# Kernel optimization log

Measured on AMD Instinct MI355X. Metric: run time of the kernel, lower is better.

The kernel has to match this reference:

```python
import jax, jax.numpy as jnp
import numpy as np

NUM_NODES = 50000
HIDDEN = 128
NUM_REL = 8
NUM_EDGES = 600000


def setup_inputs() -> dict:
    key = jax.random.key(0)
    ks = jax.random.split(key, 10)
    s = 1.0 / np.sqrt(HIDDEN)
    return {
        "edge_index": jax.random.randint(ks[0], (2, NUM_EDGES), 0, NUM_NODES, dtype=jnp.int32),
        "edge_type": jax.random.randint(ks[1], (NUM_EDGES,), 0, NUM_REL, dtype=jnp.int32),
        "node_emb": jax.random.normal(ks[2], (NUM_NODES, HIDDEN), jnp.float32),
        "W1": jax.random.normal(ks[3], (NUM_REL, HIDDEN, HIDDEN), jnp.float32) * s,
        "root1": jax.random.normal(ks[4], (HIDDEN, HIDDEN), jnp.float32) * s,
        "b1": jnp.zeros((HIDDEN,), jnp.float32),
        "W2": jax.random.normal(ks[5], (NUM_REL, HIDDEN, HIDDEN), jnp.float32) * s,
        "root2": jax.random.normal(ks[6], (HIDDEN, HIDDEN), jnp.float32) * s,
        "b2": jnp.zeros((HIDDEN,), jnp.float32),
    }


def rgcn_layer(x, W, root, bias, src, dst, rel):
    # PyG RGCNConv: per-relation MEAN aggregation of neighbor features,
    # transformed by relation weight, plus root transform and bias.
    N = x.shape[0]
    R = W.shape[0]
    # transform node features by every relation weight: [N, R, F]
    xw = jnp.einsum('nd,rdf->nrf', x, W)
    # per-(dst, relation) in-edge counts for mean normalization
    cnt = jnp.zeros((N, R), x.dtype).at[dst, rel].add(1.0)
    inv = 1.0 / jnp.maximum(cnt, 1.0)
    # per-edge message, normalized by destination's per-relation degree
    msg = xw[src, rel] * inv[dst, rel][:, None]  # [E, F]
    agg = jnp.zeros((N, W.shape[2]), x.dtype).at[dst].add(msg)
    return agg + x @ root + bias


def reference(edge_index, edge_type, node_emb, W1, root1, b1, W2, root2, b2):
    src, dst = edge_index[0], edge_index[1]
    h = jax.nn.relu(rgcn_layer(node_emb, W1, root1, b1, src, dst, edge_type))
    out = rgcn_layer(h, W2, root2, b2, src, dst, edge_type)
    return out
```

## Files before the change

### kernel.cpp

```cpp
#include <hip/hip_runtime.h>

#define H 128
#define RREL 8
#define NJ 9

typedef short bf16x8 __attribute__((ext_vector_type(8)));
typedef float f32x4 __attribute__((ext_vector_type(4)));
typedef unsigned short u16x8 __attribute__((ext_vector_type(8)));

static __device__ __forceinline__ unsigned short f2bf(float f) {
    unsigned int u = __float_as_uint(f);
    unsigned int r = (u + 0x7fffu + ((u >> 16) & 1u)) >> 16;
    return (unsigned short)r;
}
static __device__ __forceinline__ float bf2f(unsigned short u) {
    return __uint_as_float(((unsigned int)u) << 16);
}

__global__ void zero_kernel(int* p, long n) {
    long i = (long)blockIdx.x * blockDim.x + threadIdx.x;
    long stride = (long)gridDim.x * blockDim.x;
    for (; i < n; i += stride) p[i] = 0;
}

__global__ void count_kernel(const int* __restrict__ ei, const int* __restrict__ et,
                             int* __restrict__ cnt, int E) {
    int e = blockIdx.x * 256 + threadIdx.x;
    if (e >= E) return;
    int d = ei[E + e];
    int r = et[e];
    atomicAdd(&cnt[(size_t)d * RREL + r], 1);
}

__global__ void scan_block_kernel(const int* __restrict__ cnt, int* __restrict__ rploc,
                                  int* __restrict__ bsum, int N) {
    __shared__ int s[256];
    int t = threadIdx.x;
    int d = blockIdx.x * 256 + t;
    int v = 0;
    if (d < N) {
#pragma unroll
        for (int r = 0; r < RREL; ++r) v += cnt[(size_t)d * RREL + r];
    }
    s[t] = v;
    __syncthreads();
#pragma unroll
    for (int off = 1; off < 256; off <<= 1) {
        int u = 0;
        if (t >= off) u = s[t - off];
        __syncthreads();
        s[t] += u;
        __syncthreads();
    }
    if (d < N) rploc[d] = s[t] - v;
    if (t == 255) bsum[blockIdx.x] = s[255];
}

__global__ void scan_top_kernel(const int* __restrict__ bsum, int* __restrict__ boff, int nb) {
    __shared__ int s[256];
    int t = threadIdx.x;
    int v = (t < nb) ? bsum[t] : 0;
    s[t] = v;
    __syncthreads();
#pragma unroll
    for (int off = 1; off < 256; off <<= 1) {
        int u = 0;
        if (t >= off) u = s[t - off];
        __syncthreads();
        s[t] += u;
        __syncthreads();
    }
    boff[t] = s[t] - v;
}

__global__ void finalize_kernel(const int* __restrict__ cnt, const int* __restrict__ rploc,
                                const int* __restrict__ boff, int* __restrict__ rowptr2,
                                float* __restrict__ inv, int N) {
    int d = blockIdx.x * 256 + threadIdx.x;
    if (d >= N) return;
    int run = rploc[d] + boff[d >> 8];
#pragma unroll
    for (int r = 0; r < RREL; ++r) {
        int c = cnt[(size_t)d * RREL + r];
        rowptr2[(size_t)d * RREL + r] = run;
        inv[(size_t)d * RREL + r] = 1.0f / (float)max(c, 1);
        run += c;
    }
    if (d == N - 1) rowptr2[(size_t)N * RREL] = run;
}

__global__ void fill_kernel(const int* __restrict__ ei, const int* __restrict__ et,
                            int* __restrict__ cursor, const int* __restrict__ rowptr2,
                            int* __restrict__ ssrc, int E) {
    int e = blockIdx.x * 256 + threadIdx.x;
    if (e >= E) return;
    int d = ei[E + e];
    int r = et[e];
    int bin = d * RREL + r;
    int pos = rowptr2[bin] + atomicAdd(&cursor[bin], 1);
    ssrc[pos] = ei[e];
}

__global__ void tobf_kernel(const float* __restrict__ x, unsigned short* __restrict__ xb, long n) {
    long i = (long)blockIdx.x * blockDim.x + threadIdx.x;
    long stride = (long)gridDim.x * blockDim.x;
    for (; i < n; i += stride) xb[i] = f2bf(x[i]);
}

__global__ void wcat_kernel(const float* __restrict__ W1, const float* __restrict__ r1,
                            const float* __restrict__ W2, const float* __restrict__ r2,
                            unsigned short* __restrict__ WTa1, unsigned short* __restrict__ WTa2) {
    int id = blockIdx.x * 256 + threadIdx.x;
    const int per = NJ * H * H;
    if (id >= 2 * per) return;
    int b = id / per;
    int rem = id - b * per;
    int j = rem / (H * H);
    int fk = rem - j * (H * H);
    int f = fk >> 7, k = fk & 127;
    const float* W = b ? W2 : W1;
    const float* rt = b ? r2 : r1;
    float v = (j < RREL) ? W[((size_t)j * H + k) * H + f] : rt[(size_t)k * H + f];
    (b ? WTa2 : WTa1)[((size_t)j * H + f) * H + k] = f2bf(v);
}

__global__ __launch_bounds__(256) void xw_kernel(const unsigned short* __restrict__ xin,
                                                 const unsigned short* __restrict__ WTa,
                                                 unsigned short* __restrict__ Y,
                                                 int N, int j0, int j1) {
    __shared__ unsigned short Xs[64][136];
    __shared__ unsigned short Ws[128][136];
    const int t = threadIdx.x;
    const int w = t >> 6, l = t & 63;
    const int m_base = blockIdx.x * 64;
    const int colb = l & 15, quad = l >> 4;
    const u16x8 uz = {0, 0, 0, 0, 0, 0, 0, 0};
    const f32x4 fz = {0.f, 0.f, 0.f, 0.f};

#pragma unroll
    for (int p = 0; p < 4; ++p) {
        int c = p * 256 + t;
        int row = c >> 4, k8 = (c & 15) * 8;
        int gn = m_base + row;
        u16x8 v = uz;
        if (gn < N) v = *(const u16x8*)&xin[(size_t)gn * H + k8];
        *(u16x8*)&Xs[row][k8] = v;
    }

    for (int j = j0; j < j1; ++j) {
        __syncthreads();
#pragma unroll
        for (int p = 0; p < 8; ++p) {
            int c = p * 256 + t;
            int f = c >> 4, k8 = (c & 15) * 8;
            *(u16x8*)&Ws[f][k8] = *(const u16x8*)&WTa[((size_t)j * H + f) * H + k8];
        }
        __syncthreads();
        f32x4 acc[8];
#pragma unroll
        for (int n = 0; n < 8; ++n) acc[n] = fz;
#pragma unroll
        for (int ks = 0; ks < 4; ++ks) {
            int kl = ks * 32 + quad * 8;
            bf16x8 a = *(const bf16x8*)&Xs[w * 16 + colb][kl];
#pragma unroll
            for (int n = 0; n < 8; ++n) {
                bf16x8 b = *(const bf16x8*)&Ws[n * 16 + colb][kl];
                acc[n] = __builtin_amdgcn_mfma_f32_16x16x32_bf16(a, b, acc[n], 0, 0, 0);
            }
        }
        unsigned short* Yj = Y + (size_t)(j - j0) * N * H;
#pragma unroll
        for (int n = 0; n < 8; ++n) {
            int col = n * 16 + colb;
#pragma unroll
            for (int i = 0; i < 4; ++i) {
                int gn = m_base + w * 16 + quad * 4 + i;
                if (gn < N) Yj[(size_t)gn * H + col] = f2bf(acc[n][i]);
            }
        }
    }
}

__global__ __launch_bounds__(256) void gather_kernel(const unsigned short* __restrict__ Y,
                                                     const float* __restrict__ inv,
                                                     const int* __restrict__ rowptr2,
                                                     const int* __restrict__ ssrc,
                                                     const float* __restrict__ bias,
                                                     float* __restrict__ accf,
                                                     float* __restrict__ outf,
                                                     unsigned short* __restrict__ outb,
                                                     int N, int relu, int j0, int j1, int final_pass) {
    const int t = threadIdx.x;
    const int l = t & 63;
    int d = blockIdx.x * 16 + (t >> 4);
    if (d >= N) return;
    const int fl = l & 15;
    const int kc = fl * 8;
    int rp = 0;
    float ivl = 0.f;
    if (fl < 9) rp = rowptr2[(size_t)d * RREL + fl];
    if (fl < 8) ivl = inv[(size_t)d * RREL + fl];
    const int gbase = l & 48;
    float tot[8] = {};
    int rend = (j1 < RREL) ? j1 : RREL;
    for (int r = j0; r < rend; ++r) {
        int beg = __shfl(rp, gbase + r);
        int end = __shfl(rp, gbase + r + 1);
        float iv = __shfl(ivl, gbase + r);
        const unsigned short* Yr = Y + (size_t)(r - j0) * N * H;
        float af[8] = {};
        int i = beg;
        for (; i + 1 < end; i += 2) {
            int s0 = ssrc[i];
            int s1 = ssrc[i + 1];
            u16x8 v0 = *(const u16x8*)&Yr[(size_t)s0 * H + kc];
            u16x8 v1 = *(const u16x8*)&Yr[(size_t)s1 * H + kc];
#pragma unroll
            for (int j = 0; j < 8; ++j)
                af[j] += bf2f((unsigned short)v0[j]) + bf2f((unsigned short)v1[j]);
        }
        if (i < end) {
            int s0 = ssrc[i];
            u16x8 v0 = *(const u16x8*)&Yr[(size_t)s0 * H + kc];
#pragma unroll
            for (int j = 0; j < 8; ++j) af[j] += bf2f((unsigned short)v0[j]);
        }
#pragma unroll
        for (int j = 0; j < 8; ++j) tot[j] += af[j] * iv;
    }
    if (j1 == NJ) {
        u16x8 vr = *(const u16x8*)&Y[((size_t)(RREL - j0) * N + d) * H + kc];
#pragma unroll
        for (int j = 0; j < 8; ++j) tot[j] += bf2f((unsigned short)vr[j]);
    }
    if (j0 > 0) {
        f32x4 p0 = *(const f32x4*)&accf[(size_t)d * H + kc];
        f32x4 p1 = *(const f32x4*)&accf[(size_t)d * H + kc + 4];
#pragma unroll
        for (int j = 0; j < 4; ++j) { tot[j] += p0[j]; tot[4 + j] += p1[j]; }
    }
    if (final_pass) {
        f32x4 b0 = *(const f32x4*)&bias[kc];
        f32x4 b1 = *(const f32x4*)&bias[kc + 4];
#pragma unroll
        for (int j = 0; j < 4; ++j) { tot[j] += b0[j]; tot[4 + j] += b1[j]; }
        if (relu) {
#pragma unroll
            for (int j = 0; j < 8; ++j) tot[j] = fmaxf(tot[j], 0.f);
        }
        if (outf) {
            f32x4 o0, o1;
#pragma unroll
            for (int j = 0; j < 4; ++j) { o0[j] = tot[j]; o1[j] = tot[4 + j]; }
            *(f32x4*)&outf[(size_t)d * H + kc] = o0;
            *(f32x4*)&outf[(size_t)d * H + kc + 4] = o1;
        } else {
            u16x8 o;
#pragma unroll
            for (int j = 0; j < 8; ++j) o[j] = f2bf(tot[j]);
            *(u16x8*)&outb[(size_t)d * H + kc] = o;
        }
    } else {
        f32x4 o0, o1;
#pragma unroll
        for (int j = 0; j < 4; ++j) { o0[j] = tot[j]; o1[j] = tot[4 + j]; }
        *(f32x4*)&accf[(size_t)d * H + kc] = o0;
        *(f32x4*)&accf[(size_t)d * H + kc + 4] = o1;
    }
}

extern "C" void kernel_launch(void* const* d_in, const int* in_sizes, int n_in,
                              void* d_out, int out_size, void* d_ws, size_t ws_size,
                              hipStream_t stream) {
    const int* edge_index = (const int*)d_in[0];
    const int* edge_type  = (const int*)d_in[1];
    const float* node_emb = (const float*)d_in[2];
    const float* W1    = (const float*)d_in[3];
    const float* root1 = (const float*)d_in[4];
    const float* b1    = (const float*)d_in[5];
    const float* W2    = (const float*)d_in[6];
    const float* root2 = (const float*)d_in[7];
    const float* b2    = (const float*)d_in[8];
    float* out = (float*)d_out;

    const int E = in_sizes[1];
    const int N = in_sizes[2] / H;

    char* base = (char*)d_ws;
    size_t off = 0;
    auto take = [&](size_t bytes) { size_t o = off; off = (off + bytes + 63) & ~(size_t)63; return o; };
    int*   cnt     = (int*)  (base + take((size_t)N * RREL * 4));
    int*   cursor  = (int*)  (base + take((size_t)N * RREL * 4));
    int*   rploc   = (int*)  (base + take((size_t)N * 4));
    int*   bsum    = (int*)  (base + take(256 * 4));
    int*   boff    = (int*)  (base + take(256 * 4));
    int*   rowptr2 = (int*)  (base + take(((size_t)N * RREL + 1) * 4));
    float* inv     = (float*)(base + take((size_t)N * RREL * 4));
    int*   ssrc    = (int*)  (base + take((size_t)E * 4));
    unsigned short* WTa1 = (unsigned short*)(base + take((size_t)NJ * H * H * 2));
    unsigned short* WTa2 = (unsigned short*)(base + take((size_t)NJ * H * H * 2));
    unsigned short* xb  = (unsigned short*)(base + take((size_t)N * H * 2));
    unsigned short* hb  = (unsigned short*)(base + take((size_t)N * H * 2));

    size_t fixed_off = off;
    unsigned short* Y;
    float* accf = nullptr;
    int rc;
    size_t availA = (ws_size > fixed_off) ? ws_size - fixed_off : 0;
    if (availA >= (size_t)NJ * N * H * 2) {
        Y = (unsigned short*)(base + fixed_off);
        rc = NJ;
    } else {
        accf = (float*)(base + fixed_off);
        size_t off2 = fixed_off + (((size_t)N * H * 4 + 63) & ~(size_t)63);
        Y = (unsigned short*)(base + off2);
        size_t availB = (ws_size > off2) ? ws_size - off2 : 0;
        rc = (int)(availB / ((size_t)N * H * 2));
        if (rc > RREL) rc = RREL;
        if (rc < 1) rc = 1;
    }

    const int nbScan = (N + 255) / 256;

    zero_kernel<<<512, 256, 0, stream>>>(cnt, (long)N * RREL * 2);
    count_kernel<<<(E + 255) / 256, 256, 0, stream>>>(edge_index, edge_type, cnt, E);
    scan_block_kernel<<<nbScan, 256, 0, stream>>>(cnt, rploc, bsum, N);
    scan_top_kernel<<<1, 256, 0, stream>>>(bsum, boff, nbScan);
    finalize_kernel<<<nbScan, 256, 0, stream>>>(cnt, rploc, boff, rowptr2, inv, N);
    fill_kernel<<<(E + 255) / 256, 256, 0, stream>>>(edge_index, edge_type, cursor, rowptr2, ssrc, E);
    wcat_kernel<<<(2 * NJ * H * H + 255) / 256, 256, 0, stream>>>(W1, root1, W2, root2, WTa1, WTa2);
    tobf_kernel<<<1024, 256, 0, stream>>>(node_emb, xb, (long)N * H);

    const int gx = (N + 63) / 64;
    const int gg = (N + 15) / 16;

    auto run_layer = [&](const unsigned short* xin, const unsigned short* WTa, const float* bias,
                         float* of, unsigned short* ob, int relu) {
        for (int j0 = 0; j0 < NJ; j0 += rc) {
            int j1 = (j0 + rc < NJ) ? j0 + rc : NJ;
            int fin = (j1 == NJ);
            xw_kernel<<<gx, 256, 0, stream>>>(xin, WTa, Y, N, j0, j1);
            gather_kernel<<<gg, 256, 0, stream>>>(Y, inv, rowptr2, ssrc, bias, accf,
                                                  fin ? of : nullptr, fin ? ob : nullptr,
                                                  N, relu, j0, j1, fin);
        }
    };

    run_layer(xb, WTa1, b1, nullptr, hb, 1);
    run_layer(hb, WTa2, b2, out, nullptr, 0);
}
```

Baseline: 332.0 us.

## Pack edges per destination with relation bits, permute feature layout, widen xw tiles

Edges are now CSR-sorted by destination only, and each entry packs the relation id into the upper bits of the source index. The gather kernel loads 16 packed edges cooperatively and broadcasts them by shuffle, applying each edge's per-relation inverse degree. This replaces the per-(node,relation) loop with its many short, divergent segments. The xw kernel now computes 128 rows per block, reading A operands straight from global memory instead of staging them in LDS, and writes Y with 16-byte vector stores. To make those stores contiguous, the hidden dimension is permuted, which is undone through the permuted second-layer weights, the permuted bias and a strided final store. The costs are a per-edge relation check, uncoalesced A-operand loads, and a more fragile implicit layout contract between the two layers.

Measured after the change: 281.5 us. -15.2%, faster.

```diff
diff --git a/kernel.cpp b/kernel.cpp
--- a/kernel.cpp
+++ b/kernel.cpp
@@ -74,31 +74,30 @@
 }
 
 __global__ void finalize_kernel(const int* __restrict__ cnt, const int* __restrict__ rploc,
-                                const int* __restrict__ boff, int* __restrict__ rowptr2,
+                                const int* __restrict__ boff, int* __restrict__ rowptr,
                                 float* __restrict__ inv, int N) {
     int d = blockIdx.x * 256 + threadIdx.x;
     if (d >= N) return;
-    int run = rploc[d] + boff[d >> 8];
+    int rp = rploc[d] + boff[d >> 8];
+    rowptr[d] = rp;
+    int deg = 0;
 #pragma unroll
     for (int r = 0; r < RREL; ++r) {
         int c = cnt[(size_t)d * RREL + r];
-        rowptr2[(size_t)d * RREL + r] = run;
         inv[(size_t)d * RREL + r] = 1.0f / (float)max(c, 1);
-        run += c;
-    }
-    if (d == N - 1) rowptr2[(size_t)N * RREL] = run;
+        deg += c;
+    }
+    if (d == N - 1) rowptr[N] = rp + deg;
 }
 
 __global__ void fill_kernel(const int* __restrict__ ei, const int* __restrict__ et,
-                            int* __restrict__ cursor, const int* __restrict__ rowptr2,
-                            int* __restrict__ ssrc, int E) {
+                            int* __restrict__ cursor, const int* __restrict__ rowptr,
+                            int* __restrict__ packed, int E) {
     int e = blockIdx.x * 256 + threadIdx.x;
     if (e >= E) return;
     int d = ei[E + e];
-    int r = et[e];
-    int bin = d * RREL + r;
-    int pos = rowptr2[bin] + atomicAdd(&cursor[bin], 1);
-    ssrc[pos] = ei[e];
+    int pos = rowptr[d] + atomicAdd(&cursor[d], 1);
+    packed[pos] = ei[e] | (et[e] << 20);
 }
 
 __global__ void tobf_kernel(const float* __restrict__ x, unsigned short* __restrict__ xb, long n) {
@@ -109,43 +108,43 @@
 
 __global__ void wcat_kernel(const float* __restrict__ W1, const float* __restrict__ r1,
                             const float* __restrict__ W2, const float* __restrict__ r2,
-                            unsigned short* __restrict__ WTa1, unsigned short* __restrict__ WTa2) {
+                            const float* __restrict__ b1, const float* __restrict__ b2,
+                            unsigned short* __restrict__ WTa1, unsigned short* __restrict__ WTa2,
+                            float* __restrict__ biasP) {
     int id = blockIdx.x * 256 + threadIdx.x;
     const int per = NJ * H * H;
-    if (id >= 2 * per) return;
-    int b = id / per;
-    int rem = id - b * per;
-    int j = rem / (H * H);
-    int fk = rem - j * (H * H);
-    int f = fk >> 7, k = fk & 127;
-    const float* W = b ? W2 : W1;
-    const float* rt = b ? r2 : r1;
-    float v = (j < RREL) ? W[((size_t)j * H + k) * H + f] : rt[(size_t)k * H + f];
-    (b ? WTa2 : WTa1)[((size_t)j * H + f) * H + k] = f2bf(v);
+    if (id < per) {
+        int j = id / (H * H);
+        int fk = id - j * (H * H);
+        int f = fk >> 7, k = fk & 127;
+        float v = (j < RREL) ? W1[((size_t)j * H + k) * H + f] : r1[(size_t)k * H + f];
+        WTa1[id] = f2bf(v);
+        int ko = (k & 7) * 16 + (k >> 3);
+        float v2 = (j < RREL) ? W2[((size_t)j * H + ko) * H + f] : r2[(size_t)ko * H + f];
+        WTa2[id] = f2bf(v2);
+    } else if (id < per + 2 * H) {
+        int c = id - per;
+        int cp = c & 127;
+        int co = (cp & 7) * 16 + (cp >> 3);
+        biasP[c] = (c < H) ? b1[co] : b2[co];
+    }
 }
 
 __global__ __launch_bounds__(256) void xw_kernel(const unsigned short* __restrict__ xin,
                                                  const unsigned short* __restrict__ WTa,
                                                  unsigned short* __restrict__ Y,
                                                  int N, int j0, int j1) {
-    __shared__ unsigned short Xs[64][136];
     __shared__ unsigned short Ws[128][136];
     const int t = threadIdx.x;
     const int w = t >> 6, l = t & 63;
-    const int m_base = blockIdx.x * 64;
+    const int m_base = blockIdx.x * 128;
     const int colb = l & 15, quad = l >> 4;
-    const u16x8 uz = {0, 0, 0, 0, 0, 0, 0, 0};
     const f32x4 fz = {0.f, 0.f, 0.f, 0.f};
 
-#pragma unroll
-    for (int p = 0; p < 4; ++p) {
-        int c = p * 256 + t;
-        int row = c >> 4, k8 = (c & 15) * 8;
-        int gn = m_base + row;
-        u16x8 v = uz;
-        if (gn < N) v = *(const u16x8*)&xin[(size_t)gn * H + k8];
-        *(u16x8*)&Xs[row][k8] = v;
-    }
+    int row0 = m_base + w * 32 + colb;
+    int row1 = row0 + 16;
+    const unsigned short* xr0 = xin + (size_t)(row0 < N ? row0 : N - 1) * H;
+    const unsigned short* xr1 = xin + (size_t)(row1 < N ? row1 : N - 1) * H;
 
     for (int j = j0; j < j1; ++j) {
         __syncthreads();
@@ -156,27 +155,35 @@
             *(u16x8*)&Ws[f][k8] = *(const u16x8*)&WTa[((size_t)j * H + f) * H + k8];
         }
         __syncthreads();
-        f32x4 acc[8];
-#pragma unroll
-        for (int n = 0; n < 8; ++n) acc[n] = fz;
+        f32x4 acc[2][8];
+#pragma unroll
+        for (int mi = 0; mi < 2; ++mi)
+#pragma unroll
+            for (int n = 0; n < 8; ++n) acc[mi][n] = fz;
 #pragma unroll
         for (int ks = 0; ks < 4; ++ks) {
             int kl = ks * 32 + quad * 8;
-            bf16x8 a = *(const bf16x8*)&Xs[w * 16 + colb][kl];
+            bf16x8 a0 = *(const bf16x8*)&xr0[kl];
+            bf16x8 a1 = *(const bf16x8*)&xr1[kl];
 #pragma unroll
             for (int n = 0; n < 8; ++n) {
                 bf16x8 b = *(const bf16x8*)&Ws[n * 16 + colb][kl];
-                acc[n] = __builtin_amdgcn_mfma_f32_16x16x32_bf16(a, b, acc[n], 0, 0, 0);
+                acc[0][n] = __builtin_amdgcn_mfma_f32_16x16x32_bf16(a0, b, acc[0][n], 0, 0, 0);
+                acc[1][n] = __builtin_amdgcn_mfma_f32_16x16x32_bf16(a1, b, acc[1][n], 0, 0, 0);
             }
         }
         unsigned short* Yj = Y + (size_t)(j - j0) * N * H;
 #pragma unroll
-        for (int n = 0; n < 8; ++n) {
-            int col = n * 16 + colb;
+        for (int mi = 0; mi < 2; ++mi) {
 #pragma unroll
             for (int i = 0; i < 4; ++i) {
-                int gn = m_base + w * 16 + quad * 4 + i;
-                if (gn < N) Yj[(size_t)gn * H + col] = f2bf(acc[n][i]);
+                int row = m_base + w * 32 + mi * 16 + quad * 4 + i;
+                if (row < N) {
+                    u16x8 o;
+#pragma unroll
+                    for (int n = 0; n < 8; ++n) o[n] = f2bf(acc[mi][n][i]);
+                    *(u16x8*)&Yj[(size_t)row * H + colb * 8] = o;
+                }
             }
         }
     }
@@ -184,9 +191,9 @@
 
 __global__ __launch_bounds__(256) void gather_kernel(const unsigned short* __restrict__ Y,
                                                      const float* __restrict__ inv,
-                                                     const int* __restrict__ rowptr2,
-                                                     const int* __restrict__ ssrc,
-                                                     const float* __restrict__ bias,
+                                                     const int* __restrict__ rowptr,
+                                                     const int* __restrict__ packed,
+                                                     const float* __restrict__ biasP,
                                                      float* __restrict__ accf,
                                                      float* __restrict__ outf,
                                                      unsigned short* __restrict__ outb,
@@ -197,37 +204,48 @@
     if (d >= N) return;
     const int fl = l & 15;
     const int kc = fl * 8;
+    const int gbase = l & 48;
     int rp = 0;
+    if (fl < 2) rp = rowptr[d + fl];
     float ivl = 0.f;
-    if (fl < 9) rp = rowptr2[(size_t)d * RREL + fl];
     if (fl < 8) ivl = inv[(size_t)d * RREL + fl];
-    const int gbase = l & 48;
+    int beg = __shfl(rp, gbase);
+    int end = __shfl(rp, gbase + 1);
+    const int jr = (j1 < RREL) ? j1 : RREL;
     float tot[8] = {};
-    int rend = (j1 < RREL) ? j1 : RREL;
-    for (int r = j0; r < rend; ++r) {
-        int beg = __shfl(rp, gbase + r);
-        int end = __shfl(rp, gbase + r + 1);
-        float iv = __shfl(ivl, gbase + r);
-        const unsigned short* Yr = Y + (size_t)(r - j0) * N * H;
-        float af[8] = {};
-        int i = beg;
-        for (; i + 1 < end; i += 2) {
-            int s0 = ssrc[i];
-            int s1 = ssrc[i + 1];
-            u16x8 v0 = *(const u16x8*)&Yr[(size_t)s0 * H + kc];
-            u16x8 v1 = *(const u16x8*)&Yr[(size_t)s1 * H + kc];
-#pragma unroll
-            for (int j = 0; j < 8; ++j)
-                af[j] += bf2f((unsigned short)v0[j]) + bf2f((unsigned short)v1[j]);
-        }
-        if (i < end) {
-            int s0 = ssrc[i];
-            u16x8 v0 = *(const u16x8*)&Yr[(size_t)s0 * H + kc];
-#pragma unroll
-            for (int j = 0; j < 8; ++j) af[j] += bf2f((unsigned short)v0[j]);
-        }
-#pragma unroll
-        for (int j = 0; j < 8; ++j) tot[j] += af[j] * iv;
+    for (int i = beg; i < end; i += 16) {
+        int pk = (i + fl < end) ? packed[i + fl] : 0;
+        int m = end - i;
+        if (m > 16) m = 16;
+        int e = 0;
+        for (; e + 1 < m; e += 2) {
+            int v0 = __shfl(pk, gbase + e);
+            int v1 = __shfl(pk, gbase + e + 1);
+            int s0 = v0 & 0xFFFFF, r0 = v0 >> 20;
+            int s1 = v1 & 0xFFFFF, r1 = v1 >> 20;
+            if (r0 >= j0 && r0 < jr) {
+                float iv = __shfl(ivl, gbase + r0);
+                u16x8 v = *(const u16x8*)&Y[((size_t)(r0 - j0) * N + s0) * H + kc];
+#pragma unroll
+                for (int j = 0; j < 8; ++j) tot[j] += iv * bf2f((unsigned short)v[j]);
+            }
+            if (r1 >= j0 && r1 < jr) {
+                float iv = __shfl(ivl, gbase + r1);
+                u16x8 v = *(const u16x8*)&Y[((size_t)(r1 - j0) * N + s1) * H + kc];
+#pragma unroll
+                for (int j = 0; j < 8; ++j) tot[j] += iv * bf2f((unsigned short)v[j]);
+            }
+        }
+        if (e < m) {
+            int v0 = __shfl(pk, gbase + e);
+            int s0 = v0 & 0xFFFFF, r0 = v0 >> 20;
+            if (r0 >= j0 && r0 < jr) {
+                float iv = __shfl(ivl, gbase + r0);
+                u16x8 v = *(const u16x8*)&Y[((size_t)(r0 - j0) * N + s0) * H + kc];
+#pragma unroll
+                for (int j = 0; j < 8; ++j) tot[j] += iv * bf2f((unsigned short)v[j]);
+            }
+        }
     }
     if (j1 == NJ) {
         u16x8 vr = *(const u16x8*)&Y[((size_t)(RREL - j0) * N + d) * H + kc];
@@ -241,8 +259,8 @@
         for (int j = 0; j < 4; ++j) { tot[j] += p0[j]; tot[4 + j] += p1[j]; }
     }
     if (final_pass) {
-        f32x4 b0 = *(const f32x4*)&bias[kc];
-        f32x4 b1 = *(const f32x4*)&bias[kc + 4];
+        f32x4 b0 = *(const f32x4*)&biasP[kc];
+        f32x4 b1 = *(const f32x4*)&biasP[kc + 4];
 #pragma unroll
         for (int j = 0; j < 4; ++j) { tot[j] += b0[j]; tot[4 + j] += b1[j]; }
         if (relu) {
@@ -250,11 +268,8 @@
             for (int j = 0; j < 8; ++j) tot[j] = fmaxf(tot[j], 0.f);
         }
         if (outf) {
-            f32x4 o0, o1;
-#pragma unroll
-            for (int j = 0; j < 4; ++j) { o0[j] = tot[j]; o1[j] = tot[4 + j]; }
-            *(f32x4*)&outf[(size_t)d * H + kc] = o0;
-            *(f32x4*)&outf[(size_t)d * H + kc + 4] = o1;
+#pragma unroll
+            for (int j = 0; j < 8; ++j) outf[(size_t)d * H + j * 16 + fl] = tot[j];
         } else {
             u16x8 o;
 #pragma unroll
@@ -291,15 +306,16 @@
     size_t off = 0;
     auto take = [&](size_t bytes) { size_t o = off; off = (off + bytes + 63) & ~(size_t)63; return o; };
     int*   cnt     = (int*)  (base + take((size_t)N * RREL * 4));
-    int*   cursor  = (int*)  (base + take((size_t)N * RREL * 4));
+    int*   cursor  = (int*)  (base + take((size_t)N * 4));
     int*   rploc   = (int*)  (base + take((size_t)N * 4));
     int*   bsum    = (int*)  (base + take(256 * 4));
     int*   boff    = (int*)  (base + take(256 * 4));
-    int*   rowptr2 = (int*)  (base + take(((size_t)N * RREL + 1) * 4));
+    int*   rowptr  = (int*)  (base + take(((size_t)N + 1) * 4));
     float* inv     = (float*)(base + take((size_t)N * RREL * 4));
-    int*   ssrc    = (int*)  (base + take((size_t)E * 4));
+    int*   packed  = (int*)  (base + take((size_t)E * 4));
     unsigned short* WTa1 = (unsigned short*)(base + take((size_t)NJ * H * H * 2));
     unsigned short* WTa2 = (unsigned short*)(base + take((size_t)NJ * H * H * 2));
+    float* biasP   = (float*)(base + take(2 * H * 4));
     unsigned short* xb  = (unsigned short*)(base + take((size_t)N * H * 2));
     unsigned short* hb  = (unsigned short*)(base + take((size_t)N * H * 2));
 
@@ -323,30 +339,31 @@
 
     const int nbScan = (N + 255) / 256;
 
-    zero_kernel<<<512, 256, 0, stream>>>(cnt, (long)N * RREL * 2);
+    zero_kernel<<<512, 256, 0, stream>>>(cnt, (long)N * (RREL + 1));
     count_kernel<<<(E + 255) / 256, 256, 0, stream>>>(edge_index, edge_type, cnt, E);
     scan_block_kernel<<<nbScan, 256, 0, stream>>>(cnt, rploc, bsum, N);
     scan_top_kernel<<<1, 256, 0, stream>>>(bsum, boff, nbScan);
-    finalize_kernel<<<nbScan, 256, 0, stream>>>(cnt, rploc, boff, rowptr2, inv, N);
-    fill_kernel<<<(E + 255) / 256, 256, 0, stream>>>(edge_index, edge_type, cursor, rowptr2, ssrc, E);
-    wcat_kernel<<<(2 * NJ * H * H + 255) / 256, 256, 0, stream>>>(W1, root1, W2, root2, WTa1, WTa2);
+    finalize_kernel<<<nbScan, 256, 0, stream>>>(cnt, rploc, boff, rowptr, inv, N);
+    fill_kernel<<<(E + 255) / 256, 256, 0, stream>>>(edge_index, edge_type, cursor, rowptr, packed, E);
+    wcat_kernel<<<(NJ * H * H + 2 * H + 255) / 256, 256, 0, stream>>>(W1, root1, W2, root2, b1, b2,
+                                                                      WTa1, WTa2, biasP);
     tobf_kernel<<<1024, 256, 0, stream>>>(node_emb, xb, (long)N * H);
 
-    const int gx = (N + 63) / 64;
+    const int gx = (N + 127) / 128;
     const int gg = (N + 15) / 16;
 
-    auto run_layer = [&](const unsigned short* xin, const unsigned short* WTa, const float* bias,
+    auto run_layer = [&](const unsigned short* xin, const unsigned short* WTa, const float* bp,
                          float* of, unsigned short* ob, int relu) {
         for (int j0 = 0; j0 < NJ; j0 += rc) {
             int j1 = (j0 + rc < NJ) ? j0 + rc : NJ;
             int fin = (j1 == NJ);
             xw_kernel<<<gx, 256, 0, stream>>>(xin, WTa, Y, N, j0, j1);
-            gather_kernel<<<gg, 256, 0, stream>>>(Y, inv, rowptr2, ssrc, bias, accf,
+            gather_kernel<<<gg, 256, 0, stream>>>(Y, inv, rowptr, packed, bp, accf,
                                                   fin ? of : nullptr, fin ? ob : nullptr,
                                                   N, relu, j0, j1, fin);
         }
     };
 
-    run_layer(xb, WTa1, b1, nullptr, hb, 1);
-    run_layer(hb, WTa2, b2, out, nullptr, 0);
-}
+    run_layer(xb, WTa1, biasP, nullptr, hb, 1);
+    run_layer(hb, WTa2, biasP + H, out, nullptr, 0);
+}
```
